# Kernel tuning notes

Measured on AMD Instinct MI355X. Metric: run time of the kernel, lower is better.

## Reference

```python
import jax, jax.numpy as jnp
import numpy as np

B, N, D, H = 8, 2048, 1024, 1024

def setup_inputs() -> dict:
    key = jax.random.key(0)
    ks = jax.random.split(key, 7)
    s = 1.0 / np.sqrt(D)
    return {
        "x": jax.random.normal(ks[0], (B, N, D), dtype=jnp.float32),
        "Wq": jax.random.uniform(ks[1], (D, H), jnp.float32, -s, s),
        "bq": jax.random.uniform(ks[2], (H,), jnp.float32, -s, s),
        "Wk": jax.random.uniform(ks[3], (D, H), jnp.float32, -s, s),
        "bk": jax.random.uniform(ks[4], (H,), jnp.float32, -s, s),
        "Wv": jax.random.uniform(ks[5], (D, H), jnp.float32, -s, s),
        "bv": jax.random.uniform(ks[6], (H,), jnp.float32, -s, s),
    }

def reference(x, Wq, bq, Wk, bk, Wv, bv):
    # q, k, v: [B, N, H]
    q = jnp.einsum('bnd,dh->bnh', x, Wq) + bq
    k = jnp.einsum('bnd,dh->bnh', x, Wk) + bk
    v = jnp.einsum('bnd,dh->bnh', x, Wv) + bv
    scale = 1.0 / jnp.sqrt(jnp.asarray(q.shape[-1], q.dtype))
    score = jnp.einsum('bqh,bkh->bqk', q, k) * scale  # [B, N, N]
    causal = jnp.tril(jnp.ones((q.shape[1], q.shape[1]), dtype=bool))
    score = jnp.where(causal, score, -jnp.inf)
    attn = jax.nn.softmax(score, axis=-1)
    # dropout p=0.0 -> identity (deterministic reference)
    return jnp.einsum('bqk,bkh->bqh', attn, v)
```

## Files before the change

### kernel.cpp

```cpp
#include <hip/hip_runtime.h>
#include <hip/hip_bf16.h>
#include <stdint.h>

#define BB 8
#define NN 2048
#define DD 1024
#define HH 1024

using f32x4 = __attribute__((ext_vector_type(4))) float;
using s16x8 = __attribute__((ext_vector_type(8))) short;

__device__ __forceinline__ short f2bf(float f){
  union { float f; uint32_t u; } v; v.f = f;
  uint32_t r = (v.u + 0x7fffu + ((v.u >> 16) & 1u)) >> 16;
  return (short)r;
}
__device__ __forceinline__ float bf2f(short s){
  union { uint32_t u; float f; } v; v.u = ((uint32_t)(uint16_t)s) << 16; return v.f;
}

#define MFMA(a,b,c) __builtin_amdgcn_mfma_f32_16x16x32_bf16((a),(b),(c),0,0,0)

#define GL16(gp, lp) __builtin_amdgcn_global_load_lds( \
    (const __attribute__((address_space(1))) void*)(gp), \
    (__attribute__((address_space(3))) void*)(lp), 16, 0, 0)

__global__ __launch_bounds__(256) void k_conv_x(const float* __restrict__ x,
                                                short* __restrict__ xb){
  int gid = blockIdx.x*256 + threadIdx.x;
  const float4* xv = (const float4*)x;
  float4 a = xv[(size_t)gid*2], b2 = xv[(size_t)gid*2+1];
  s16x8 o;
  o[0]=f2bf(a.x);  o[1]=f2bf(a.y);  o[2]=f2bf(a.z);  o[3]=f2bf(a.w);
  o[4]=f2bf(b2.x); o[5]=f2bf(b2.y); o[6]=f2bf(b2.z); o[7]=f2bf(b2.w);
  *(s16x8*)(xb + (size_t)gid*8) = o;
}

__global__ __launch_bounds__(256) void k_conv_w(const float* __restrict__ Wq,
                                                const float* __restrict__ Wk,
                                                const float* __restrict__ Wv,
                                                short* __restrict__ Wt){
  __shared__ float tile[64][65];
  int bx = blockIdx.x; int mat = bx >> 8; int ti = bx & 255;
  int d0 = (ti >> 4) << 6, h0 = (ti & 15) << 6;
  const float* W = (mat==0) ? Wq : (mat==1 ? Wk : Wv);
  int t = threadIdx.x;
  for (int i=0;i<16;i++){ int e = i*256 + t; int r = e>>6, c = e&63;
    tile[r][c] = W[(size_t)(d0+r)*HH + h0 + c]; }
  __syncthreads();
  for (int i=0;i<16;i++){ int e = i*256 + t; int r = e>>6, c = e&63;
    Wt[(size_t)(mat*HH + h0 + r)*DD + d0 + c] = f2bf(tile[c][r]); }
}

__global__ __launch_bounds__(256) void k_gemm(const short* __restrict__ Aw,
                                              const short* __restrict__ Bw,
                                              const float* __restrict__ bq,
                                              const float* __restrict__ bk,
                                              const float* __restrict__ bv,
                                              short* __restrict__ Qw,
                                              short* __restrict__ Kw,
                                              short* __restrict__ Vt){
  __shared__ short Al[128*32];
  __shared__ short Bl[128*32];
  int t = threadIdx.x; int l = t & 63; int w = t >> 6;
  int bn = blockIdx.x, bm = blockIdx.y;
  int m0 = bm << 7, c0 = bn << 7;
  f32x4 acc[4][4] = {};
  int soff = w*2048 + l*16;
  int rA0 = ((w>>1)*64 + (l&15))*32 + (l>>4)*8;
  int rB0 = ((w&1)*64 + (l&15))*32 + (l>>4)*8;
  for (int k0 = 0; k0 < DD; k0 += 32){
    __syncthreads();
    #pragma unroll
    for (int j=0;j<2;j++){
      int off = soff + j*1024;
      int row = off >> 6, ke = (off & 63) >> 1;
      GL16(Aw + (size_t)(m0+row)*DD + k0 + ke, ((char*)Al) + off);
      GL16(Bw + (size_t)(c0+row)*DD + k0 + ke, ((char*)Bl) + off);
    }
    __syncthreads();
    s16x8 af[4], bf[4];
    #pragma unroll
    for (int i=0;i<4;i++){
      af[i] = *(const s16x8*)&Al[rA0 + i*512];
      bf[i] = *(const s16x8*)&Bl[rB0 + i*512];
    }
    #pragma unroll
    for (int mi=0;mi<4;mi++)
      #pragma unroll
      for (int ni=0;ni<4;ni++)
        acc[mi][ni] = MFMA(af[mi], bf[ni], acc[mi][ni]);
  }
  int wr = w>>1, wc = w&1;
  int rg_base = m0 + wr*64;
  int cg_base = c0 + wc*64;
  int mat = cg_base >> 10;
  const float* bias = (mat==0) ? bq : (mat==1 ? bk : bv);
  #pragma unroll
  for (int ni=0;ni<4;ni++){
    int cg = cg_base + ni*16 + (l&15);
    int cin = cg & 1023;
    float bval = bias[cin];
    #pragma unroll
    for (int mi=0;mi<4;mi++){
      int rg = rg_base + mi*16 + (l>>4)*4;
      #pragma unroll
      for (int i=0;i<4;i++){
        short val = f2bf(acc[mi][ni][i] + bval);
        int row = rg + i;
        if (mat==0)      Qw[(size_t)row*HH + cin] = val;
        else if (mat==1) Kw[(size_t)row*HH + cin] = val;
        else {
          int bb = row >> 11, n = row & 2047;
          Vt[((size_t)bb*HH + cin)*NN + n] = val;
        }
      }
    }
  }
}

__global__ __launch_bounds__(256) void k_s(const short* __restrict__ Qw,
                                           const short* __restrict__ Kw,
                                           short* __restrict__ Pp){
  __shared__ short Al[128*32];
  __shared__ short Bl[128*32];
  int t = threadIdx.x; int l = t & 63; int w = t >> 6;
  int p = blockIdx.x; int b = p & 7; int ti = p >> 3;
  int tr = 0; while ((tr+1)*(tr+2)/2 <= ti) tr++;
  int tc = ti - tr*(tr+1)/2;
  const short* Aq = Qw + ((size_t)b*NN + tr*128)*HH;
  const short* Bk = Kw + ((size_t)b*NN + tc*128)*HH;
  const float SC_EXP = 0.04508422002783268f;
  f32x4 acc[4][4] = {};
  int soff = w*2048 + l*16;
  int rA0 = ((w>>1)*64 + (l&15))*32 + (l>>4)*8;
  int rB0 = ((w&1)*64 + (l&15))*32 + (l>>4)*8;
  for (int k0 = 0; k0 < DD; k0 += 32){
    __syncthreads();
    #pragma unroll
    for (int j=0;j<2;j++){
      int off = soff + j*1024;
      int row = off >> 6, ke = (off & 63) >> 1;
      GL16(Aq + (size_t)row*HH + k0 + ke, ((char*)Al) + off);
      GL16(Bk + (size_t)row*HH + k0 + ke, ((char*)Bl) + off);
    }
    __syncthreads();
    s16x8 af[4], bf[4];
    #pragma unroll
    for (int i=0;i<4;i++){
      af[i] = *(const s16x8*)&Al[rA0 + i*512];
      bf[i] = *(const s16x8*)&Bl[rB0 + i*512];
    }
    #pragma unroll
    for (int mi=0;mi<4;mi++)
      #pragma unroll
      for (int ni=0;ni<4;ni++)
        acc[mi][ni] = MFMA(af[mi], bf[ni], acc[mi][ni]);
  }
  short* Pt = Pp + ((size_t)b*136 + ti)*16384;
  int wr = w>>1, wc = w&1;
  #pragma unroll
  for (int mi=0;mi<4;mi++){
    #pragma unroll
    for (int ni=0;ni<4;ni++){
      int cl = wc*64 + ni*16 + (l&15);
      #pragma unroll
      for (int i=0;i<4;i++){
        int rl = wr*64 + mi*16 + (l>>4)*4 + i;
        bool keep = (tc*128 + cl) <= (tr*128 + rl);
        float pv = keep ? exp2f(acc[mi][ni][i]*SC_EXP) : 0.f;
        Pt[rl*128 + cl] = f2bf(pv);
      }
    }
  }
}

__global__ __launch_bounds__(256) void k_pv(const short* __restrict__ Pp,
                                            const short* __restrict__ Vt,
                                            float* __restrict__ out){
  __shared__ short Al[128*32];
  __shared__ short Bl[128*32];
  int t = threadIdx.x; int l = t & 63; int w = t >> 6;
  int p = blockIdx.x; int b = p & 7, hc = (p>>3) & 7, tr = p >> 6;
  const short* Pb = Pp + ((size_t)b*136 + tr*(tr+1)/2)*16384;
  const short* Bv = Vt + ((size_t)b*HH + hc*128)*NN;
  f32x4 acc[4][4] = {};
  float ls[4] = {0.f,0.f,0.f,0.f};
  int soff = w*2048 + l*16;
  int rA0 = ((w>>1)*64 + (l&15))*32 + (l>>4)*8;
  int rB0 = ((w&1)*64 + (l&15))*32 + (l>>4)*8;
  const int KE = (tr+1)*128;
  for (int k0 = 0; k0 < KE; k0 += 32){
    __syncthreads();
    const short* At = Pb + (size_t)(k0>>7)*16384 + (k0 & 96);
    #pragma unroll
    for (int j=0;j<2;j++){
      int off = soff + j*1024;
      int row = off >> 6, ke = (off & 63) >> 1;
      GL16(At + row*128 + ke, ((char*)Al) + off);
      GL16(Bv + (size_t)row*NN + k0 + ke, ((char*)Bl) + off);
    }
    __syncthreads();
    s16x8 af[4], bf[4];
    #pragma unroll
    for (int i=0;i<4;i++){
      af[i] = *(const s16x8*)&Al[rA0 + i*512];
      bf[i] = *(const s16x8*)&Bl[rB0 + i*512];
    }
    #pragma unroll
    for (int mi=0;mi<4;mi++){
      #pragma unroll
      for (int e=0;e<8;e++) ls[mi] += bf2f(af[mi][e]);
    }
    #pragma unroll
    for (int mi=0;mi<4;mi++)
      #pragma unroll
      for (int ni=0;ni<4;ni++)
        acc[mi][ni] = MFMA(af[mi], bf[ni], acc[mi][ni]);
  }
  #pragma unroll
  for (int mi=0;mi<4;mi++){
    ls[mi] += __shfl_xor(ls[mi], 16);
    ls[mi] += __shfl_xor(ls[mi], 32);
  }
  int wr = w>>1, wc = w&1;
  int g = l >> 4, c = l & 15;
  #pragma unroll
  for (int mi=0;mi<4;mi++){
    float linv[4];
    #pragma unroll
    for (int i=0;i<4;i++) linv[i] = 1.0f / __shfl(ls[mi], g*4 + i);
    #pragma unroll
    for (int ni=0;ni<4;ni++){
      int cl = wc*64 + ni*16 + c;
      #pragma unroll
      for (int i=0;i<4;i++){
        int rl = wr*64 + mi*16 + g*4 + i;
        out[((size_t)(b*NN + tr*128 + rl))*HH + hc*128 + cl] = acc[mi][ni][i]*linv[i];
      }
    }
  }
}

extern "C" void kernel_launch(void* const* d_in, const int* in_sizes, int n_in,
                              void* d_out, int out_size, void* d_ws, size_t ws_size,
                              hipStream_t stream) {
  const float* x  = (const float*)d_in[0];
  const float* Wq = (const float*)d_in[1];
  const float* bq = (const float*)d_in[2];
  const float* Wk = (const float*)d_in[3];
  const float* bk = (const float*)d_in[4];
  const float* Wv = (const float*)d_in[5];
  const float* bv = (const float*)d_in[6];
  char* ws = (char*)d_ws;
  short* xb = (short*)(ws);
  short* Pp = (short*)(ws);
  short* Wt = (short*)(ws + 35651584u);
  short* Qw = (short*)(ws + 41943040u);
  short* Kw = (short*)(ws + 75497472u);
  short* Vt = (short*)(ws + 109051904u);

  k_conv_x<<<8192, 256, 0, stream>>>(x, xb);
  k_conv_w<<<768, 256, 0, stream>>>(Wq, Wk, Wv, Wt);
  k_gemm<<<dim3(24,128), 256, 0, stream>>>(xb, Wt, bq, bk, bv, Qw, Kw, Vt);
  k_s<<<1088, 256, 0, stream>>>(Qw, Kw, Pp);
  k_pv<<<1024, 256, 0, stream>>>(Pp, Vt, (float*)d_out);
}
```

Before: 313.3 us.

## Rewrite QKV projection GEMM with 256x256 double-buffered swizzled tiles and separate V transpose

The QKV projection GEMM moves from 128x128 tiles with k-step 32 to 256x256 tiles with 512 threads and k-step 64. It double-buffers LDS with an XOR-swizzled layout, interleaves async global-to-LDS prefetch of the next tile with MFMA on the current one, and raises wave priority around the MFMA blocks. The strided transposed store of V inside the GEMM epilogue is replaced by a plain row-major store plus a separate tiled transpose kernel. This trades an extra pass over V and more LDS per block for better operand reuse, overlapped loads and coalesced epilogue writes.

```diff
diff --git a/kernel.cpp b/kernel.cpp
--- a/kernel.cpp
+++ b/kernel.cpp
@@ -52,71 +52,113 @@
     Wt[(size_t)(mat*HH + h0 + r)*DD + d0 + c] = f2bf(tile[c][r]); }
 }
 
-__global__ __launch_bounds__(256) void k_gemm(const short* __restrict__ Aw,
-                                              const short* __restrict__ Bw,
-                                              const float* __restrict__ bq,
-                                              const float* __restrict__ bk,
-                                              const float* __restrict__ bv,
-                                              short* __restrict__ Qw,
-                                              short* __restrict__ Kw,
-                                              short* __restrict__ Vt){
-  __shared__ short Al[128*32];
-  __shared__ short Bl[128*32];
-  int t = threadIdx.x; int l = t & 63; int w = t >> 6;
-  int bn = blockIdx.x, bm = blockIdx.y;
-  int m0 = bm << 7, c0 = bn << 7;
-  f32x4 acc[4][4] = {};
-  int soff = w*2048 + l*16;
-  int rA0 = ((w>>1)*64 + (l&15))*32 + (l>>4)*8;
-  int rB0 = ((w&1)*64 + (l&15))*32 + (l>>4)*8;
-  for (int k0 = 0; k0 < DD; k0 += 32){
-    __syncthreads();
-    #pragma unroll
-    for (int j=0;j<2;j++){
-      int off = soff + j*1024;
-      int row = off >> 6, ke = (off & 63) >> 1;
-      GL16(Aw + (size_t)(m0+row)*DD + k0 + ke, ((char*)Al) + off);
-      GL16(Bw + (size_t)(c0+row)*DD + k0 + ke, ((char*)Bl) + off);
-    }
-    __syncthreads();
-    s16x8 af[4], bf[4];
-    #pragma unroll
-    for (int i=0;i<4;i++){
-      af[i] = *(const s16x8*)&Al[rA0 + i*512];
-      bf[i] = *(const s16x8*)&Bl[rB0 + i*512];
-    }
-    #pragma unroll
-    for (int mi=0;mi<4;mi++)
-      #pragma unroll
-      for (int ni=0;ni<4;ni++)
-        acc[mi][ni] = MFMA(af[mi], bf[ni], acc[mi][ni]);
-  }
-  int wr = w>>1, wc = w&1;
-  int rg_base = m0 + wr*64;
-  int cg_base = c0 + wc*64;
-  int mat = cg_base >> 10;
+__global__ __launch_bounds__(512,2) void k_gemm(const short* __restrict__ Aw,
+                                                const short* __restrict__ Bw,
+                                                const float* __restrict__ bq,
+                                                const float* __restrict__ bk,
+                                                const float* __restrict__ bv,
+                                                short* __restrict__ Qw,
+                                                short* __restrict__ Kw,
+                                                short* __restrict__ Vw){
+  __shared__ short Al[2][256*64];
+  __shared__ short Bl[2][256*64];
+  const int t = threadIdx.x, l = t & 63, w = t >> 6;
+  const int g = l >> 4, c = l & 15;
+  const int bn = blockIdx.x, bm = blockIdx.y;
+  const int m0 = bm << 8, c0 = bn << 8;
+  const int wr = w >> 2, wc = w & 3;
+  f32x4 acc[8][4] = {};
+
+  const int srow = l >> 3, schunk = l & 7;
+  auto stageA = [&](int kt, int bf, int j){
+    int row = j*64 + w*8 + srow;
+    int u = schunk ^ (row & 7);
+    GL16(Aw + (size_t)(m0+row)*DD + kt*64 + u*8,
+         ((char*)&Al[bf][0]) + (j*64 + w*8)*128);
+  };
+  auto stageB = [&](int kt, int bf, int j){
+    int row = j*64 + w*8 + srow;
+    int u = schunk ^ (row & 7);
+    GL16(Bw + (size_t)(c0+row)*DD + kt*64 + u*8,
+         ((char*)&Bl[bf][0]) + (j*64 + w*8)*128);
+  };
+
+  #pragma unroll
+  for (int j=0;j<4;j++){ stageA(0,0,j); stageB(0,0,j); }
+  __syncthreads();
+
+  for (int kt = 0; kt < 16; ++kt){
+    const int bf = kt & 1;
+    const bool pf = (kt < 15);
+    #pragma unroll
+    for (int p = 0; p < 4; ++p){
+      s16x8 af[2][2], bfr[4][2];
+      #pragma unroll
+      for (int mi2=0;mi2<2;mi2++){
+        int row = wr*128 + (p*2+mi2)*16 + c;
+        #pragma unroll
+        for (int kk=0;kk<2;kk++)
+          af[mi2][kk] = *(const s16x8*)&Al[bf][row*64 + (((kk*4+g)^(row&7))*8)];
+      }
+      #pragma unroll
+      for (int ni=0;ni<4;ni++){
+        int row = wc*64 + ni*16 + c;
+        #pragma unroll
+        for (int kk=0;kk<2;kk++)
+          bfr[ni][kk] = *(const s16x8*)&Bl[bf][row*64 + (((kk*4+g)^(row&7))*8)];
+      }
+      if (pf){
+        if      (p==0){ stageA(kt+1,bf^1,0); stageB(kt+1,bf^1,0); stageA(kt+1,bf^1,1); }
+        else if (p==1){ stageB(kt+1,bf^1,1); stageA(kt+1,bf^1,2); stageB(kt+1,bf^1,2); }
+        else if (p==2){ stageA(kt+1,bf^1,3); stageB(kt+1,bf^1,3); }
+      }
+      __builtin_amdgcn_s_barrier();
+      __builtin_amdgcn_s_setprio(1);
+      #pragma unroll
+      for (int mi2=0;mi2<2;mi2++)
+        #pragma unroll
+        for (int ni=0;ni<4;ni++)
+          #pragma unroll
+          for (int kk=0;kk<2;kk++)
+            acc[p*2+mi2][ni] = MFMA(af[mi2][kk], bfr[ni][kk], acc[p*2+mi2][ni]);
+      __builtin_amdgcn_s_setprio(0);
+      if (p < 3) __builtin_amdgcn_s_barrier();
+    }
+    asm volatile("s_waitcnt vmcnt(0)" ::: "memory");
+    __builtin_amdgcn_s_barrier();
+  }
+
+  const int mat = bn >> 2;
+  short* Outp = (mat==0) ? Qw : (mat==1 ? Kw : Vw);
   const float* bias = (mat==0) ? bq : (mat==1 ? bk : bv);
+  const int colbase = (bn & 3)*256 + wc*64;
   #pragma unroll
   for (int ni=0;ni<4;ni++){
-    int cg = cg_base + ni*16 + (l&15);
-    int cin = cg & 1023;
+    int cin = colbase + ni*16 + c;
     float bval = bias[cin];
     #pragma unroll
-    for (int mi=0;mi<4;mi++){
-      int rg = rg_base + mi*16 + (l>>4)*4;
-      #pragma unroll
-      for (int i=0;i<4;i++){
-        short val = f2bf(acc[mi][ni][i] + bval);
-        int row = rg + i;
-        if (mat==0)      Qw[(size_t)row*HH + cin] = val;
-        else if (mat==1) Kw[(size_t)row*HH + cin] = val;
-        else {
-          int bb = row >> 11, n = row & 2047;
-          Vt[((size_t)bb*HH + cin)*NN + n] = val;
-        }
-      }
-    }
-  }
+    for (int mi=0;mi<8;mi++){
+      int rg = m0 + wr*128 + mi*16 + g*4;
+      #pragma unroll
+      for (int i=0;i<4;i++)
+        Outp[(size_t)(rg+i)*HH + cin] = f2bf(acc[mi][ni][i] + bval);
+    }
+  }
+}
+
+__global__ __launch_bounds__(256) void k_vtrans(const short* __restrict__ Vw,
+                                                short* __restrict__ Vt){
+  __shared__ uint16_t tile[64][65];
+  int bx = blockIdx.x; int b = bx >> 9; int rem = bx & 511;
+  int n0 = (rem >> 4) << 6, h0 = (rem & 15) << 6;
+  int t = threadIdx.x;
+  const uint16_t* vin = (const uint16_t*)Vw;
+  uint16_t* vout = (uint16_t*)Vt;
+  for (int i=0;i<16;i++){ int e = i*256 + t; int r = e>>6, c = e&63;
+    tile[r][c] = vin[((size_t)b*NN + n0 + r)*HH + h0 + c]; }
+  __syncthreads();
+  for (int i=0;i<16;i++){ int e = i*256 + t; int r = e>>6, c = e&63;
+    vout[((size_t)b*HH + h0 + r)*NN + n0 + c] = tile[c][r]; }
 }
 
 __global__ __launch_bounds__(256) void k_s(const short* __restrict__ Qw,
@@ -255,14 +297,16 @@
   char* ws = (char*)d_ws;
   short* xb = (short*)(ws);
   short* Pp = (short*)(ws);
-  short* Wt = (short*)(ws + 35651584u);
-  short* Qw = (short*)(ws + 41943040u);
-  short* Kw = (short*)(ws + 75497472u);
-  short* Vt = (short*)(ws + 109051904u);
+  short* Wt = (short*)(ws + 33554432u);
+  short* Qw = (short*)(ws + 39845888u);
+  short* Kw = (short*)(ws + 73400320u);
+  short* Vw = (short*)(ws + 106954752u);
+  short* Vt = (short*)(ws + 140509184u);
 
   k_conv_x<<<8192, 256, 0, stream>>>(x, xb);
   k_conv_w<<<768, 256, 0, stream>>>(Wq, Wk, Wv, Wt);
-  k_gemm<<<dim3(24,128), 256, 0, stream>>>(xb, Wt, bq, bk, bv, Qw, Kw, Vt);
+  k_gemm<<<dim3(12,64), 512, 0, stream>>>(xb, Wt, bq, bk, bv, Qw, Kw, Vw);
+  k_vtrans<<<4096, 256, 0, stream>>>(Vw, Vt);
   k_s<<<1088, 256, 0, stream>>>(Qw, Kw, Pp);
   k_pv<<<1024, 256, 0, stream>>>(Pp, Vt, (float*)d_out);
 }
```

Result: faster. 286.9 us (-8.4%).
